# Performance work log

Measured on AMD Instinct MI355X. Metric: run time of the kernel, lower is better.

The kernel has to match this reference:

```python
import jax, jax.numpy as jnp
import numpy as np

N = 100000      # nodes
E = 1600000     # edges (avg degree 16)
EMB = 128
L = 3           # num_layers
NUM_OPS = 64
MAX_BW = 64     # max_bitwidth
P = 4           # max_num_params


def setup_inputs() -> dict:
    key = jax.random.key(0)
    ks = jax.random.split(key, 24)
    w = lambda k, s: jax.random.normal(k, s, jnp.float32) * 0.05
    return {
        "ops": jax.random.randint(ks[0], (N,), 0, NUM_OPS),
        "params": jax.random.randint(ks[1], (N, P), 0, MAX_BW),
        "edge_src": jax.random.randint(ks[2], (E,), 0, N),
        "edge_dst": jax.random.randint(ks[3], (E,), 0, N),
        "op_emb_table": w(ks[4], (NUM_OPS, EMB)),
        "param_emb_table": w(ks[5], (MAX_BW, EMB)),
        "opmlp_w1": w(ks[6], ((1 + P) * EMB, EMB)), "opmlp_b1": w(ks[7], (EMB,)),
        "opmlp_w2": w(ks[8], (EMB, EMB)), "opmlp_b2": w(ks[9], (EMB,)),
        "conv_w": w(ks[10], (L, EMB, EMB)), "conv_b": w(ks[11], (L, EMB)),
        "mlp_w1": w(ks[12], (L * EMB, EMB)), "mlp_b1": w(ks[13], (EMB,)),
        "mlp_w2": w(ks[14], (EMB, EMB)), "mlp_b2": w(ks[15], (EMB,)),
        "mlpinv_w1": w(ks[16], (L * EMB, EMB)), "mlpinv_b1": w(ks[17], (EMB,)),
        "mlpinv_w2": w(ks[18], (EMB, EMB)), "mlpinv_b2": w(ks[19], (EMB,)),
        "comb_w": w(ks[20], (2 * EMB, EMB)), "comb_b": w(ks[21], (EMB,)),
    }


def _lrelu(x):
    return jax.nn.leaky_relu(x)  # slope 0.01, matches nn.LeakyReLU default


def _gin_mean(feat, src, dst, w, b):
    # DGL GINConv(aggregator='mean', eps=0): apply_func(feat + mean_in_neighbors(feat))
    n = feat.shape[0]
    msg = jax.ops.segment_sum(feat[src], dst, num_segments=n)           # [N, EMB]
    deg = jax.ops.segment_sum(jnp.ones(src.shape, feat.dtype), dst, num_segments=n)
    agg = msg / jnp.maximum(deg, 1.0)[:, None]
    return _lrelu((feat + agg) @ w + b)


def reference(ops, params, edge_src, edge_dst,
              op_emb_table, param_emb_table,
              opmlp_w1, opmlp_b1, opmlp_w2, opmlp_b2,
              conv_w, conv_b,
              mlp_w1, mlp_b1, mlp_w2, mlp_b2,
              mlpinv_w1, mlpinv_b1, mlpinv_w2, mlpinv_b2,
              comb_w, comb_b):
    n = ops.shape[0]
    # OpEmb: cat([op_emb] + per-param embs) -> MLP
    op_e = op_emb_table[ops]                               # [N, EMB]
    par_e = param_emb_table[params].reshape(n, -1)         # [N, P*EMB]
    h = jnp.concatenate([op_e, par_e], axis=1)
    h = _lrelu(h @ opmlp_w1 + opmlp_b1) @ opmlp_w2 + opmlp_b2
    states = h
    states_inv = h  # op_emb called twice on same inputs in the original

    conv_outs = []
    for i in range(L):
        states = _gin_mean(states, edge_src, edge_dst, conv_w[i], conv_b[i])
        conv_outs.append(states.sum(axis=0))
    final_sum = states.sum(axis=0)

    conv_outs_inv = []
    for i in range(L):
        states_inv = _gin_mean(states_inv, edge_dst, edge_src, conv_w[i], conv_b[i])
        # NOTE: original code appends states.sum(dim=0) (the final forward states),
        # not states_inv -- faithfully reproduced.
        conv_outs_inv.append(final_sum)

    g_emb = _lrelu(jnp.concatenate(conv_outs) @ mlp_w1 + mlp_b1) @ mlp_w2 + mlp_b2
    g_inv_emb = _lrelu(jnp.concatenate(conv_outs_inv) @ mlpinv_w1 + mlpinv_b1) @ mlpinv_w2 + mlpinv_b2

    out1 = jnp.concatenate([g_emb, g_inv_emb]) @ comb_w + comb_b          # [EMB]
    out2 = jnp.concatenate([states, states_inv], axis=1) @ comb_w + comb_b  # [N, EMB]
    return (out1, out2)
```

## Files before the change

### kernel.cpp

```cpp
#include <hip/hip_runtime.h>


typedef unsigned int  uint;
typedef unsigned short ushort;
typedef float  f32x4  __attribute__((ext_vector_type(4)));
typedef short  bf16x8 __attribute__((ext_vector_type(8)));

#define ABITS 9
#define CAPB  12288
#define CHUNK 2048

__device__ __forceinline__ float lrelu(float x) { return x > 0.0f ? x : 0.01f * x; }
__device__ __forceinline__ ushort f2b(float x) {
    uint u = __float_as_uint(x);
    return (ushort)((u + 0x7fffu + ((u >> 16) & 1u)) >> 16);
}
__device__ __forceinline__ float lof(uint u) { return __uint_as_float(u << 16); }
__device__ __forceinline__ float hif(uint u) { return __uint_as_float(u & 0xffff0000u); }

__global__ __launch_bounds__(256) void buildprep_kernel(
    const int* __restrict__ esrc, const int* __restrict__ edst, int E, int nb, int nChunks,
    int* __restrict__ gcur, uint2* __restrict__ binbuf,
    const float* __restrict__ opT, const float* __restrict__ parT,
    const float* __restrict__ W1, float* __restrict__ Atab,
    const float* __restrict__ convw, const float* __restrict__ ow2,
    const float* __restrict__ cw, ushort* __restrict__ Wt)
{
    __shared__ int hist[448];
    __shared__ int lstart[448];
    __shared__ int gbase[448];
    __shared__ int lcur[448];
    __shared__ int gsum[8];
    __shared__ uint sKey[CHUNK * 2];
    __shared__ uint sPay[CHUNK * 2];
    __shared__ ushort sBin[CHUNK * 2];
    int tid = threadIdx.x, lane = tid & 63;

    if ((int)blockIdx.x >= nChunks) {
        int rb = (int)blockIdx.x - nChunks;
        if (rb < 160) {
            int b = (rb << 1) | (tid >> 7);
            int t = b >> 6, v = b & 63, j = tid & 127;
            const float* emb = (t == 0 ? opT : parT) + v * 128;
            const float* w = W1 + (size_t)t * 128 * 128;
            float acc = 0.f;
            for (int k = 0; k < 128; ++k) acc += emb[k] * w[k * 128 + j];
            Atab[(size_t)b * 128 + j] = acc;
        } else {
            int t = (rb - 160) * 256 + tid;
            int img = t >> 14, idx = t & 16383;
            int k = idx >> 7, c = idx & 127;
            const float* src;
            if (img < 3)       src = convw + img * 16384;
            else if (img == 3) src = ow2;
            else               src = cw + (img - 4) * 16384;
            float v = src[k * 128 + c];
            int byteoff = (img << 15) + (c << 8) + ((((k >> 3) ^ (c & 7)) << 4)) + ((k & 7) << 1);
            Wt[byteoff >> 1] = f2b(v);
        }
        return;
    }

    int nb2 = nb * 2;
    int base = (int)blockIdx.x * CHUNK;
    int cnt = min(CHUNK, E - base);
    for (int i = tid; i < 448; i += 256) hist[i] = 0;
    __syncthreads();
    int s[8], d[8];
    #pragma unroll
    for (int i = 0; i < 8; ++i) {
        int idx = i * 256 + tid;
        if (idx < cnt) {
            s[i] = esrc[base + idx];
            d[i] = edst[base + idx];
            atomicAdd(&hist[d[i] >> ABITS], 1);
            atomicAdd(&hist[nb + (s[i] >> ABITS)], 1);
        } else s[i] = -1;
    }
    __syncthreads();
    #pragma unroll
    for (int k = 0; k < 2; ++k) {
        int idx = k * 256 + tid;
        int v = (idx < 448) ? hist[idx] : 0;
        int p = v;
        #pragma unroll
        for (int sh = 1; sh < 64; sh <<= 1) { int t = __shfl_up(p, sh, 64); if (lane >= sh) p += t; }
        if (idx < 448) {
            lstart[idx] = p - v;
            if (lane == 63) gsum[idx >> 6] = p;
        }
    }
    __syncthreads();
    if (tid == 0) { int run = 0; for (int g = 0; g < 7; ++g) { int t = gsum[g]; gsum[g] = run; run += t; } }
    __syncthreads();
    #pragma unroll
    for (int k = 0; k < 2; ++k) {
        int idx = k * 256 + tid;
        if (idx < 448) lstart[idx] += gsum[idx >> 6];
    }
    __syncthreads();
    for (int i = tid; i < nb2; i += 256) {
        int h = hist[i];
        gbase[i] = h ? atomicAdd(&gcur[i], h) : 0;
        lcur[i] = lstart[i];
    }
    __syncthreads();
    #pragma unroll
    for (int i = 0; i < 8; ++i) {
        if (s[i] >= 0) {
            int bf = d[i] >> ABITS;
            int p = atomicAdd(&lcur[bf], 1);
            sKey[p] = (uint)d[i]; sPay[p] = (uint)s[i]; sBin[p] = (ushort)bf;
            int bi = nb + (s[i] >> ABITS);
            int q = atomicAdd(&lcur[bi], 1);
            sKey[q] = (uint)s[i]; sPay[q] = (uint)d[i]; sBin[q] = (ushort)bi;
        }
    }
    __syncthreads();
    int total = 2 * cnt;
    for (int p = tid; p < total; p += 256) {
        int b = sBin[p];
        int pos = gbase[b] + (p - lstart[b]);
        if (pos < CAPB) binbuf[(size_t)b * CAPB + pos] = make_uint2(sKey[p], sPay[p]);
    }
}

__device__ __forceinline__ void stage_w(const ushort* __restrict__ img, ushort* ldsW, int tid)
{
    const uint4* s = (const uint4*)img;
    uint4* d = (uint4*)ldsW;
    #pragma unroll
    for (int i = 0; i < 4; ++i) d[tid + (i << 9)] = s[tid + (i << 9)];
}

__global__ __launch_bounds__(512, 2) void mid_kernel(
    const uint2* __restrict__ binbuf, const int* __restrict__ gcur, int nb, int N,
    int* __restrict__ csr_f, int* __restrict__ off_f, int* __restrict__ cnt_f,
    int* __restrict__ csr_i, int* __restrict__ off_i, int* __restrict__ cnt_i,
    const int* __restrict__ ops, const int* __restrict__ params,
    const float* __restrict__ Atab, const float* __restrict__ b1,
    const ushort* __restrict__ W2img, const float* __restrict__ b2,
    ushort* __restrict__ S0)
{
    __shared__ __align__(16) ushort ldsW[16384];
    __shared__ __align__(16) ushort ldsA[16384];
    int tid = threadIdx.x, lane = tid & 63, w = tid >> 6;
    int nb2 = 2 * nb;

    if ((int)blockIdx.x < nb2) {
        int* hist = (int*)ldsA;
        int* cur  = hist + 512;
        int* gsum = cur + 512;
        int b = blockIdx.x;
        int dir = (b >= nb) ? 1 : 0;
        int binLocal = dir ? b - nb : b;
        int node0 = binLocal << ABITS;
        int nn = min(512, N - node0);
        int total = min(gcur[b], CAPB);
        const uint2* seg = binbuf + (size_t)b * CAPB;
        int* csr = dir ? csr_i : csr_f;
        int* off = dir ? off_i : off_f;
        int* cnt = dir ? cnt_i : cnt_f;

        hist[tid] = 0;
        __syncthreads();
        for (int e = tid; e < total; e += 512) {
            uint2 kp = seg[e];
            atomicAdd(&hist[kp.x - (uint)node0], 1);
        }
        __syncthreads();
        int v = hist[tid];
        int p = v;
        #pragma unroll
        for (int sh = 1; sh < 64; sh <<= 1) { int t = __shfl_up(p, sh, 64); if (lane >= sh) p += t; }
        if (lane == 63) gsum[w] = p;
        __syncthreads();
        if (tid == 0) { int run = 0; for (int g = 0; g < 8; ++g) { int t = gsum[g]; gsum[g] = run; run += t; } }
        __syncthreads();
        int lv = p - v + gsum[w];
        cur[tid] = lv;
        int csrBase = binLocal * CAPB;
        if (tid < nn) { off[node0 + tid] = csrBase + lv; cnt[node0 + tid] = v; }
        __syncthreads();
        int* csrSeg = csr + csrBase;
        for (int e = tid; e < total; e += 512) {
            uint2 kp = seg[e];
            int q = atomicAdd(&cur[kp.x - (uint)node0], 1);
            csrSeg[q] = (int)(kp.y << 8);
        }
        return;
    }

    int node0 = ((int)blockIdx.x - nb2) << 7;
    stage_w(W2img, ldsW, tid);

    int r = tid >> 2, sub = tid & 3;
    int g = node0 + r;
    float4 acc4[8];
    if (g < N) {
        int op = ops[g];
        const float4* T = (const float4*)(Atab + ((size_t)op << 7) + (sub << 5));
        #pragma unroll
        for (int q = 0; q < 8; ++q) acc4[q] = T[q];
        #pragma unroll
        for (int p = 0; p < 4; ++p) {
            int pv = params[(g << 2) + p];
            const float4* Tp = (const float4*)(Atab + ((size_t)((p + 1) * 64 + pv) << 7) + (sub << 5));
            #pragma unroll
            for (int q = 0; q < 8; ++q) {
                float4 u = Tp[q];
                acc4[q].x += u.x; acc4[q].y += u.y; acc4[q].z += u.z; acc4[q].w += u.w;
            }
        }
        const float4* Bv = (const float4*)(b1 + (sub << 5));
        #pragma unroll
        for (int q = 0; q < 8; ++q) {
            float4 bb = Bv[q];
            acc4[q].x = lrelu(acc4[q].x + bb.x);
            acc4[q].y = lrelu(acc4[q].y + bb.y);
            acc4[q].z = lrelu(acc4[q].z + bb.z);
            acc4[q].w = lrelu(acc4[q].w + bb.w);
        }
    } else {
        #pragma unroll
        for (int q = 0; q < 8; ++q) acc4[q] = make_float4(0.f, 0.f, 0.f, 0.f);
    }
    int akey = r & 7;
    #pragma unroll
    for (int q2 = 0; q2 < 4; ++q2) {
        int ch = (sub << 2) + q2;
        float4 a = acc4[q2 * 2], b = acc4[q2 * 2 + 1];
        uint4 pk;
        pk.x = (uint)f2b(a.x) | ((uint)f2b(a.y) << 16);
        pk.y = (uint)f2b(a.z) | ((uint)f2b(a.w) << 16);
        pk.z = (uint)f2b(b.x) | ((uint)f2b(b.y) << 16);
        pk.w = (uint)f2b(b.z) | ((uint)f2b(b.w) << 16);
        *(uint4*)((char*)ldsA + r * 256 + ((ch ^ akey) << 4)) = pk;
    }
    __syncthreads();

    int l15 = lane & 15, lg = lane >> 4;
    int node = node0 + (w << 4) + l15;
    int brow = (w << 4) + l15;
    const char* Bb = (const char*)ldsA + brow * 256;
    int bkey = (brow & 7) << 4;
    f32x4 acc[8];
    #pragma unroll
    for (int i = 0; i < 8; ++i) acc[i] = f32x4{0.f, 0.f, 0.f, 0.f};
    #pragma unroll
    for (int kk = 0; kk < 4; ++kk) {
        bf16x8 bfr = *(const bf16x8*)(Bb + ((((kk << 2) + lg) << 4) ^ bkey));
        #pragma unroll
        for (int ct = 0; ct < 8; ++ct) {
            int c = (ct << 4) + l15;
            const char* Ab = (const char*)ldsW + c * 256;
            bf16x8 af = *(const bf16x8*)(Ab + ((((kk << 2) + lg) << 4) ^ ((c & 7) << 4)));
            acc[ct] = __builtin_amdgcn_mfma_f32_16x16x32_bf16(af, bfr, acc[ct], 0, 0, 0);
        }
    }
    if (node < N) {
        #pragma unroll
        for (int ct = 0; ct < 8; ++ct) {
            int ch0 = (ct << 4) + (lg << 2);
            float4 bb = *(const float4*)(b2 + ch0);
            uint2 pk;
            pk.x = (uint)f2b(acc[ct][0] + bb.x) | ((uint)f2b(acc[ct][1] + bb.y) << 16);
            pk.y = (uint)f2b(acc[ct][2] + bb.z) | ((uint)f2b(acc[ct][3] + bb.w) << 16);
            *(uint2*)((char*)S0 + ((size_t)node << 8) + (ch0 << 1)) = pk;
        }
    }
}

__global__ __launch_bounds__(256, 8) void glayer_kernel(
    const ushort* __restrict__ Sf_in, const ushort* __restrict__ Si_in,
    ushort* __restrict__ Sf_out, ushort* __restrict__ Si_out,
    const int* __restrict__ csr_f, const int* __restrict__ off_f, const int* __restrict__ cnt_f,
    const int* __restrict__ csr_i, const int* __restrict__ off_i, const int* __restrict__ cnt_i,
    const ushort* __restrict__ Wimg, const float* __restrict__ bias,
    float* __restrict__ colsumR, int nBlkF, int N)
{
    __shared__ __align__(16) char msgL[16 * 272];
    __shared__ float ldsCS[128];
    int tid = threadIdx.x, lane = tid & 63, w = tid >> 6;
    bool fwd = (int)blockIdx.x < nBlkF;
    int blkLocal = fwd ? (int)blockIdx.x : (int)blockIdx.x - nBlkF;
    const char* Sp = (const char*)(fwd ? Sf_in : Si_in);
    ushort* Sout = fwd ? Sf_out : Si_out;
    const int* csr  = fwd ? csr_f : csr_i;
    const int* offA = fwd ? off_f : off_i;
    const int* cntA = fwd ? cnt_f : cnt_i;

    if (tid < 128) ldsCS[tid] = 0.f;

    int half = lane >> 5;
    int lb = (lane & 31) << 3;
    int node0 = blkLocal << 4;

    #pragma unroll
    for (int i = 0; i < 4; ++i) {
        int g = node0 + (w << 2) + i;
        float a0 = 0.f, a1 = 0.f, a2 = 0.f, a3 = 0.f;
        if (g < N) {
            int off = offA[g], deg = cntA[g];
            int d = 0;
            for (; d + 8 <= deg; d += 8) {
                int b0 = csr[off + d + 0 + half];
                int b1 = csr[off + d + 2 + half];
                int b2 = csr[off + d + 4 + half];
                int b3 = csr[off + d + 6 + half];
                uint2 v0 = *(const uint2*)(Sp + (uint)(b0 + lb));
                uint2 v1 = *(const uint2*)(Sp + (uint)(b1 + lb));
                uint2 v2 = *(const uint2*)(Sp + (uint)(b2 + lb));
                uint2 v3 = *(const uint2*)(Sp + (uint)(b3 + lb));
                a0 += (lof(v0.x) + lof(v1.x)) + (lof(v2.x) + lof(v3.x));
                a1 += (hif(v0.x) + hif(v1.x)) + (hif(v2.x) + hif(v3.x));
                a2 += (lof(v0.y) + lof(v1.y)) + (lof(v2.y) + lof(v3.y));
                a3 += (hif(v0.y) + hif(v1.y)) + (hif(v2.y) + hif(v3.y));
            }
            for (; d + 2 <= deg; d += 2) {
                int b = csr[off + d + half];
                uint2 v = *(const uint2*)(Sp + (uint)(b + lb));
                a0 += lof(v.x); a1 += hif(v.x); a2 += lof(v.y); a3 += hif(v.y);
            }
            if (d < deg && half == 0) {
                int b = csr[off + d];
                uint2 v = *(const uint2*)(Sp + (uint)(b + lb));
                a0 += lof(v.x); a1 += hif(v.x); a2 += lof(v.y); a3 += hif(v.y);
            }
            a0 += __shfl_xor(a0, 32);
            a1 += __shfl_xor(a1, 32);
            a2 += __shfl_xor(a2, 32);
            a3 += __shfl_xor(a3, 32);
            float iv = 1.0f / fmaxf((float)deg, 1.0f);
            uint2 self = *(const uint2*)(Sp + ((size_t)g << 8) + lb);
            a0 = lof(self.x) + a0 * iv;
            a1 = hif(self.x) + a1 * iv;
            a2 = lof(self.y) + a2 * iv;
            a3 = hif(self.y) + a3 * iv;
        }
        if (half == 0) {
            uint2 pk;
            pk.x = (uint)f2b(a0) | ((uint)f2b(a1) << 16);
            pk.y = (uint)f2b(a2) | ((uint)f2b(a3) << 16);
            *(uint2*)(msgL + ((w << 2) + i) * 272 + lb) = pk;
        }
    }
    __syncthreads();

    int l15 = lane & 15, lg = lane >> 4;
    const char* Bb = msgL + l15 * 272;
    f32x4 acc0 = f32x4{0.f, 0.f, 0.f, 0.f};
    f32x4 acc1 = f32x4{0.f, 0.f, 0.f, 0.f};
    int ct0 = w << 1;
    int c0 = (ct0 << 4) + l15;
    int c1 = ((ct0 + 1) << 4) + l15;
    const char* A0 = (const char*)Wimg + c0 * 256;
    const char* A1 = (const char*)Wimg + c1 * 256;
    int k0 = (c0 & 7) << 4, k1 = (c1 & 7) << 4;
    #pragma unroll
    for (int kk = 0; kk < 4; ++kk) {
        int chk = ((kk << 2) + lg) << 4;
        bf16x8 bfr = *(const bf16x8*)(Bb + chk);
        bf16x8 af0 = *(const bf16x8*)(A0 + (chk ^ k0));
        bf16x8 af1 = *(const bf16x8*)(A1 + (chk ^ k1));
        acc0 = __builtin_amdgcn_mfma_f32_16x16x32_bf16(af0, bfr, acc0, 0, 0, 0);
        acc1 = __builtin_amdgcn_mfma_f32_16x16x32_bf16(af1, bfr, acc1, 0, 0, 0);
    }

    int gs = node0 + l15;
    bool valid = gs < N;
    #pragma unroll
    for (int q = 0; q < 2; ++q) {
        f32x4 a = q ? acc1 : acc0;
        int ch0 = ((ct0 + q) << 4) + (lg << 2);
        float4 bb = *(const float4*)(bias + ch0);
        float o0 = lrelu(a[0] + bb.x);
        float o1 = lrelu(a[1] + bb.y);
        float o2 = lrelu(a[2] + bb.z);
        float o3 = lrelu(a[3] + bb.w);
        if (valid) {
            uint2 pk;
            pk.x = (uint)f2b(o0) | ((uint)f2b(o1) << 16);
            pk.y = (uint)f2b(o2) | ((uint)f2b(o3) << 16);
            *(uint2*)((char*)Sout + ((size_t)gs << 8) + (ch0 << 1)) = pk;
        }
        if (fwd) {
            float s0 = valid ? o0 : 0.f, s1 = valid ? o1 : 0.f;
            float s2 = valid ? o2 : 0.f, s3 = valid ? o3 : 0.f;
            #pragma unroll
            for (int m = 1; m < 16; m <<= 1) {
                s0 += __shfl_xor(s0, m);
                s1 += __shfl_xor(s1, m);
                s2 += __shfl_xor(s2, m);
                s3 += __shfl_xor(s3, m);
            }
            if (l15 == 0) {
                atomicAdd(&ldsCS[ch0 + 0], s0);
                atomicAdd(&ldsCS[ch0 + 1], s1);
                atomicAdd(&ldsCS[ch0 + 2], s2);
                atomicAdd(&ldsCS[ch0 + 3], s3);
            }
        }
    }
    if (fwd) {
        __syncthreads();
        if (tid < 128) atomicAdd(&colsumR[(((int)blockIdx.x & 7) << 7) + tid], ldsCS[tid]);
    }
}

__device__ __forceinline__ void final_body(
    float* lds, const float* __restrict__ convsum,
    const float* __restrict__ mw1, const float* __restrict__ mb1,
    const float* __restrict__ mw2, const float* __restrict__ mb2,
    const float* __restrict__ iw1, const float* __restrict__ ib1,
    const float* __restrict__ iw2, const float* __restrict__ ib2,
    const float* __restrict__ cw, const float* __restrict__ cb,
    float* __restrict__ out1)
{
    float* x  = lds;
    float* pa = lds + 384;
    float* pb = lds + 896;
    float* t1 = lds + 1408;
    float* t2 = lds + 1536;
    int tid = threadIdx.x, j = tid & 127, s = tid >> 7;
    if (tid < 384) {
        const float* cs = convsum + (((size_t)(tid >> 7)) << 10) + (tid & 127);
        float acc = 0.f;
        #pragma unroll
        for (int r = 0; r < 8; ++r) acc += cs[r << 7];
        x[tid] = acc;
    }
    __syncthreads();
    float a = 0.f, c = 0.f;
    for (int k = s * 96; k < s * 96 + 96; ++k) {
        a += x[k] * mw1[k * 128 + j];
        c += x[256 + (k & 127)] * iw1[k * 128 + j];
    }
    pa[tid] = a; pb[tid] = c;
    __syncthreads();
    if (s == 0) {
        t1[j] = lrelu(pa[j] + pa[128 + j] + pa[256 + j] + pa[384 + j] + mb1[j]);
        t2[j] = lrelu(pb[j] + pb[128 + j] + pb[256 + j] + pb[384 + j] + ib1[j]);
    }
    __syncthreads();
    float b = 0.f, d = 0.f;
    for (int k = s * 32; k < s * 32 + 32; ++k) {
        b += t1[k] * mw2[k * 128 + j];
        d += t2[k] * iw2[k * 128 + j];
    }
    pa[tid] = b; pb[tid] = d;
    __syncthreads();
    if (s == 0) {
        t1[j] = pa[j] + pa[128 + j] + pa[256 + j] + pa[384 + j] + mb2[j];
        t2[j] = pb[j] + pb[128 + j] + pb[256 + j] + pb[384 + j] + ib2[j];
    }
    __syncthreads();
    float e = 0.f;
    for (int k = s * 32; k < s * 32 + 32; ++k)
        e += t1[k] * cw[k * 128 + j] + t2[k] * cw[(128 + k) * 128 + j];
    pa[tid] = e;
    __syncthreads();
    if (s == 0) out1[j] = pa[j] + pa[128 + j] + pa[256 + j] + pa[384 + j] + cb[j];
}

__global__ __launch_bounds__(512, 4) void out2_fused(
    const ushort* __restrict__ Sf, const ushort* __restrict__ Si,
    const ushort* __restrict__ CWimg, const float* __restrict__ cb,
    float* __restrict__ out, int gemmBlocks, int N,
    const float* __restrict__ convsum,
    const float* __restrict__ mw1, const float* __restrict__ mb1,
    const float* __restrict__ mw2, const float* __restrict__ mb2,
    const float* __restrict__ iw1, const float* __restrict__ ib1,
    const float* __restrict__ iw2, const float* __restrict__ ib2,
    const float* __restrict__ cw, float* __restrict__ out1)
{
    __shared__ __align__(16) ushort ldsW[16384];
    int tid = threadIdx.x, lane = tid & 63, w = tid >> 6;
    if ((int)blockIdx.x >= gemmBlocks) {
        final_body((float*)ldsW, convsum, mw1, mb1, mw2, mb2,
                   iw1, ib1, iw2, ib2, cw, cb, out1);
        return;
    }
    int node0 = blockIdx.x << 7;
    int l15 = lane & 15, lg = lane >> 4;
    int node = node0 + (w << 4) + l15;
    int gr = min(node, N - 1);
    f32x4 acc[8];
    #pragma unroll
    for (int i = 0; i < 8; ++i) acc[i] = f32x4{0.f, 0.f, 0.f, 0.f};
    #pragma unroll
    for (int pass = 0; pass < 2; ++pass) {
        if (pass) __syncthreads();
        stage_w(CWimg + (pass << 14), ldsW, tid);
        __syncthreads();
        const char* Bb = (const char*)(pass ? Si : Sf) + ((size_t)gr << 8);
        #pragma unroll
        for (int kk = 0; kk < 4; ++kk) {
            bf16x8 bfr = *(const bf16x8*)(Bb + (((kk << 2) + lg) << 4));
            #pragma unroll
            for (int ct = 0; ct < 8; ++ct) {
                int c = (ct << 4) + l15;
                const char* Ab = (const char*)ldsW + c * 256;
                bf16x8 af = *(const bf16x8*)(Ab + ((((kk << 2) + lg) << 4) ^ ((c & 7) << 4)));
                acc[ct] = __builtin_amdgcn_mfma_f32_16x16x32_bf16(af, bfr, acc[ct], 0, 0, 0);
            }
        }
    }
    if (node < N) {
        #pragma unroll
        for (int ct = 0; ct < 8; ++ct) {
            int ch0 = (ct << 4) + (lg << 2);
            float4 bb = *(const float4*)(cb + ch0);
            float4 o;
            o.x = acc[ct][0] + bb.x;
            o.y = acc[ct][1] + bb.y;
            o.z = acc[ct][2] + bb.z;
            o.w = acc[ct][3] + bb.w;
            *(float4*)(out + (size_t)node * 128 + ch0) = o;
        }
    }
}

extern "C" void kernel_launch(void* const* d_in, const int* in_sizes, int n_in,
                              void* d_out, int out_size, void* d_ws, size_t ws_size,
                              hipStream_t stream)
{
    (void)n_in; (void)out_size; (void)ws_size;
    const int*   ops    = (const int*)d_in[0];
    const int*   params = (const int*)d_in[1];
    const int*   esrc   = (const int*)d_in[2];
    const int*   edst   = (const int*)d_in[3];
    const float* opT    = (const float*)d_in[4];
    const float* parT   = (const float*)d_in[5];
    const float* ow1    = (const float*)d_in[6];
    const float* ob1    = (const float*)d_in[7];
    const float* ow2    = (const float*)d_in[8];
    const float* ob2    = (const float*)d_in[9];
    const float* convw  = (const float*)d_in[10];
    const float* convb  = (const float*)d_in[11];
    const float* mw1    = (const float*)d_in[12];
    const float* mb1    = (const float*)d_in[13];
    const float* mw2    = (const float*)d_in[14];
    const float* mb2    = (const float*)d_in[15];
    const float* iw1    = (const float*)d_in[16];
    const float* ib1    = (const float*)d_in[17];
    const float* iw2    = (const float*)d_in[18];
    const float* ib2    = (const float*)d_in[19];
    const float* cw     = (const float*)d_in[20];
    const float* cb     = (const float*)d_in[21];

    const int N = in_sizes[0];
    const int E = in_sizes[2];
    const int nb = (N + 511) >> ABITS;
    const size_t NP = (size_t)N * 128;

    ushort* S0   = (ushort*)d_ws;
    ushort* S1   = S0 + NP;
    ushort* S2   = S1 + NP;
    ushort* S3   = S2 + NP;
    ushort* Wt   = S3 + NP;
    float*  Atab = (float*)(Wt + 6 * 16384);
    float*  convsum = Atab + 320 * 128;
    int*    gcur = (int*)(convsum + 3072);
    uint2*  binbuf = (uint2*)(gcur + 512);
    int*    csr_f = (int*)(binbuf + (size_t)2 * nb * CAPB);
    int*    csr_i = csr_f + (size_t)nb * CAPB;
    int*    off_f = csr_i + (size_t)nb * CAPB;
    int*    cnt_f = off_f + N;
    int*    off_i = cnt_f + N;
    int*    cnt_i = off_i + N;

    float* out1 = (float*)d_out;
    float* out2 = out1 + 128;

    hipMemsetAsync(convsum, 0, sizeof(float) * 3584, stream);

    const int nChunks = (E + CHUNK - 1) / CHUNK;
    buildprep_kernel<<<nChunks + 160 + 384, 256, 0, stream>>>(
        esrc, edst, E, nb, nChunks, gcur, binbuf,
        opT, parT, ow1, Atab, convw, ow2, cw, Wt);

    const int grid = (N + 127) / 128;
    mid_kernel<<<2 * nb + grid, 512, 0, stream>>>(
        binbuf, gcur, nb, N,
        csr_f, off_f, cnt_f, csr_i, off_i, cnt_i,
        ops, params, Atab, ob1, Wt + 3 * 16384, ob2, S0);

    const int nBlkF = (N + 15) / 16;
    glayer_kernel<<<2 * nBlkF, 256, 0, stream>>>(S0, S0, S1, S3,
        csr_f, off_f, cnt_f, csr_i, off_i, cnt_i,
        Wt,             convb,       convsum,        nBlkF, N);
    glayer_kernel<<<2 * nBlkF, 256, 0, stream>>>(S1, S3, S0, S2,
        csr_f, off_f, cnt_f, csr_i, off_i, cnt_i,
        Wt + 16384,     convb + 128, convsum + 1024, nBlkF, N);
    glayer_kernel<<<2 * nBlkF, 256, 0, stream>>>(S0, S2, S1, S3,
        csr_f, off_f, cnt_f, csr_i, off_i, cnt_i,
        Wt + 2 * 16384, convb + 256, convsum + 2048, nBlkF, N);

    out2_fused<<<grid + 1, 512, 0, stream>>>(S1, S3, Wt + 4 * 16384, cb, out2, grid, N,
                                             convsum, mw1, mb1, mw2, mb2,
                                             iw1, ib1, iw2, ib2, cw, out1);
}
```

Before: 599.5 us.

## Make each wave own a 16-node tile in GIN layer, dropping block barriers

Each block in the layer kernel now covers 64 nodes instead of 16. Each wave aggregates its own 16 nodes into a private LDS slab and then runs the full 8-column-tile MFMA on them, so the block-wide __syncthreads and the LDS column-sum staging are removed. Column sums go straight to global atomics spread across 8 replica slots. In exchange each wave reloads all weight fragments, holds more accumulator registers, and issues more global atomics, and the grid has a quarter as many blocks.

```diff
diff --git a/kernel.cpp b/kernel.cpp
--- a/kernel.cpp
+++ b/kernel.cpp
@@ -279,8 +279,7 @@
     const ushort* __restrict__ Wimg, const float* __restrict__ bias,
     float* __restrict__ colsumR, int nBlkF, int N)
 {
-    __shared__ __align__(16) char msgL[16 * 272];
-    __shared__ float ldsCS[128];
+    __shared__ __align__(16) char msgL[4 * 16 * 272];
     int tid = threadIdx.x, lane = tid & 63, w = tid >> 6;
     bool fwd = (int)blockIdx.x < nBlkF;
     int blkLocal = fwd ? (int)blockIdx.x : (int)blockIdx.x - nBlkF;
@@ -290,15 +289,13 @@
     const int* offA = fwd ? off_f : off_i;
     const int* cntA = fwd ? cnt_f : cnt_i;
 
-    if (tid < 128) ldsCS[tid] = 0.f;
-
+    char* slab = msgL + w * (16 * 272);
     int half = lane >> 5;
     int lb = (lane & 31) << 3;
-    int node0 = blkLocal << 4;
-
-    #pragma unroll
-    for (int i = 0; i < 4; ++i) {
-        int g = node0 + (w << 2) + i;
+    int node0 = (blkLocal << 6) + (w << 4);
+
+    for (int i = 0; i < 16; ++i) {
+        int g = node0 + i;
         float a0 = 0.f, a1 = 0.f, a2 = 0.f, a3 = 0.f;
         if (g < N) {
             int off = offA[g], deg = cntA[g];
@@ -342,42 +339,41 @@
             uint2 pk;
             pk.x = (uint)f2b(a0) | ((uint)f2b(a1) << 16);
             pk.y = (uint)f2b(a2) | ((uint)f2b(a3) << 16);
-            *(uint2*)(msgL + ((w << 2) + i) * 272 + lb) = pk;
-        }
-    }
-    __syncthreads();
+            *(uint2*)(slab + i * 272 + lb) = pk;
+        }
+    }
+    asm volatile("s_waitcnt lgkmcnt(0)" ::: "memory");
+    __builtin_amdgcn_sched_barrier(0);
 
     int l15 = lane & 15, lg = lane >> 4;
-    const char* Bb = msgL + l15 * 272;
-    f32x4 acc0 = f32x4{0.f, 0.f, 0.f, 0.f};
-    f32x4 acc1 = f32x4{0.f, 0.f, 0.f, 0.f};
-    int ct0 = w << 1;
-    int c0 = (ct0 << 4) + l15;
-    int c1 = ((ct0 + 1) << 4) + l15;
-    const char* A0 = (const char*)Wimg + c0 * 256;
-    const char* A1 = (const char*)Wimg + c1 * 256;
-    int k0 = (c0 & 7) << 4, k1 = (c1 & 7) << 4;
+    const char* Bb = slab + l15 * 272;
+    f32x4 acc[8];
+    #pragma unroll
+    for (int i = 0; i < 8; ++i) acc[i] = f32x4{0.f, 0.f, 0.f, 0.f};
     #pragma unroll
     for (int kk = 0; kk < 4; ++kk) {
         int chk = ((kk << 2) + lg) << 4;
         bf16x8 bfr = *(const bf16x8*)(Bb + chk);
-        bf16x8 af0 = *(const bf16x8*)(A0 + (chk ^ k0));
-        bf16x8 af1 = *(const bf16x8*)(A1 + (chk ^ k1));
-        acc0 = __builtin_amdgcn_mfma_f32_16x16x32_bf16(af0, bfr, acc0, 0, 0, 0);
-        acc1 = __builtin_amdgcn_mfma_f32_16x16x32_bf16(af1, bfr, acc1, 0, 0, 0);
+        #pragma unroll
+        for (int ct = 0; ct < 8; ++ct) {
+            int c = (ct << 4) + l15;
+            const char* Ab = (const char*)Wimg + c * 256;
+            bf16x8 af = *(const bf16x8*)(Ab + (chk ^ ((c & 7) << 4)));
+            acc[ct] = __builtin_amdgcn_mfma_f32_16x16x32_bf16(af, bfr, acc[ct], 0, 0, 0);
+        }
     }
 
     int gs = node0 + l15;
     bool valid = gs < N;
-    #pragma unroll
-    for (int q = 0; q < 2; ++q) {
-        f32x4 a = q ? acc1 : acc0;
-        int ch0 = ((ct0 + q) << 4) + (lg << 2);
+    int rep = (((int)blockIdx.x << 2) | w) & 7;
+    #pragma unroll
+    for (int ct = 0; ct < 8; ++ct) {
+        int ch0 = (ct << 4) + (lg << 2);
         float4 bb = *(const float4*)(bias + ch0);
-        float o0 = lrelu(a[0] + bb.x);
-        float o1 = lrelu(a[1] + bb.y);
-        float o2 = lrelu(a[2] + bb.z);
-        float o3 = lrelu(a[3] + bb.w);
+        float o0 = lrelu(acc[ct][0] + bb.x);
+        float o1 = lrelu(acc[ct][1] + bb.y);
+        float o2 = lrelu(acc[ct][2] + bb.z);
+        float o3 = lrelu(acc[ct][3] + bb.w);
         if (valid) {
             uint2 pk;
             pk.x = (uint)f2b(o0) | ((uint)f2b(o1) << 16);
@@ -395,16 +391,13 @@
                 s3 += __shfl_xor(s3, m);
             }
             if (l15 == 0) {
-                atomicAdd(&ldsCS[ch0 + 0], s0);
-                atomicAdd(&ldsCS[ch0 + 1], s1);
-                atomicAdd(&ldsCS[ch0 + 2], s2);
-                atomicAdd(&ldsCS[ch0 + 3], s3);
-            }
-        }
-    }
-    if (fwd) {
-        __syncthreads();
-        if (tid < 128) atomicAdd(&colsumR[(((int)blockIdx.x & 7) << 7) + tid], ldsCS[tid]);
+                float* cs = colsumR + (rep << 7) + ch0;
+                atomicAdd(cs + 0, s0);
+                atomicAdd(cs + 1, s1);
+                atomicAdd(cs + 2, s2);
+                atomicAdd(cs + 3, s3);
+            }
+        }
     }
 }
 
@@ -586,7 +579,7 @@
         csr_f, off_f, cnt_f, csr_i, off_i, cnt_i,
         ops, params, Atab, ob1, Wt + 3 * 16384, ob2, S0);
 
-    const int nBlkF = (N + 15) / 16;
+    const int nBlkF = (N + 63) / 64;
     glayer_kernel<<<2 * nBlkF, 256, 0, stream>>>(S0, S0, S1, S3,
         csr_f, off_f, cnt_f, csr_i, off_i, cnt_i,
         Wt,             convb,       convsum,        nBlkF, N);
```

After: 923.6 us. +54.0%, slower.
